# Optimization experiments

Measured on AMD Instinct MI355X. Metric: run time of the kernel, lower is better.

The kernel has to match this reference:

```python
import jax, jax.numpy as jnp
import numpy as np

B, T, H, D, V = 1, 512, 12, 64, 32000  # batch, seq, heads, head_dim, vocab


def setup_inputs() -> dict:
    key = jax.random.key(0)
    k0, k1, k2, k3 = jax.random.split(key, 4)
    x = jax.random.normal(k0, (B, T, H * D), dtype=jnp.float32)
    # per-head FFN weights: torch Linear(head_dim, head_dim) -> weight (out,in)=(D,D)
    W_ffn = jax.random.normal(k1, (H, D, D), dtype=jnp.float32) * 0.02
    b_ffn = jnp.zeros((H, D), dtype=jnp.float32)
    # per-head vocab attention: torch Linear(head_dim, vocab_size, bias=False) -> weight (V,D)
    W_vocab = jax.random.normal(k2, (H, V, D), dtype=jnp.float32) * 0.02
    temps = jnp.ones((H,), dtype=jnp.float32)
    # shared vocab embedding table (vocab_size, n_embd)
    E = jax.random.normal(k3, (V, H * D), dtype=jnp.float32) * 0.02
    return {"x": x, "W_ffn": W_ffn, "b_ffn": b_ffn, "W_vocab": W_vocab,
            "temps": temps, "E": E}


def reference(x, W_ffn, b_ffn, W_vocab, temps, E):
    Bx, Tx, C = x.shape
    Hn, Dn, _ = W_ffn.shape
    xh = x.reshape(Bx, Tx, Hn, Dn)                         # (B,T,H,D)
    # per-head FFN (Linear: y = x @ W^T + b)
    ffn = jnp.einsum('bthd,hed->bthe', xh, W_ffn) + b_ffn  # (B,T,H,D)
    # per-head vocab logits against weight bank (H,V,D)
    logits = jnp.einsum('bthd,hvd->bthv', ffn, W_vocab)    # (B,T,H,V)
    temp = jnp.maximum(temps, 0.1)[None, None, :, None]    # clamp(min=0.1)
    w = jax.nn.softmax(logits / temp, axis=-1)             # (B,T,H,V)
    # back-project through per-head slices of vocab embedding table
    Eh = E.reshape(E.shape[0], Hn, Dn)                     # (V,H,D)
    out = jnp.einsum('bthv,vhd->bthd', w, Eh)              # (B,T,H,D)
    # dropout is identity at eval (p used at train only)
    return out.reshape(Bx, Tx, C)
```

## Files before the change

### kernel.cpp

```cpp
#include <hip/hip_runtime.h>
#include <hip/hip_bf16.h>
#include <cstddef>

#define T_TOK 512
#define NH    12
#define HD    64
#define NV    32000
#define CEMB  768
#define NC    20
#define VC    (NV/NC)
#define NSUB  (VC/64)
#define QTILE 256
#define SK 72
#define SE 72
#define SP 72

typedef short v8bf __attribute__((ext_vector_type(8)));
typedef float v4f  __attribute__((ext_vector_type(4)));

__device__ __forceinline__ unsigned short f2bf(float f) {
    unsigned u = __float_as_uint(f);
    u += 0x7fffu + ((u >> 16) & 1u);
    return (unsigned short)(u >> 16);
}

__global__ void ffn_kernel(const float* __restrict__ x, const float* __restrict__ Wf,
                           const float* __restrict__ bf, const float* __restrict__ temps,
                           unsigned short* __restrict__ Qb) {
    const int t = blockIdx.x, h = blockIdx.y, e = threadIdx.x;
    __shared__ float xs[HD];
    xs[e] = x[t*CEMB + h*HD + e];
    __syncthreads();
    const float4* w4  = (const float4*)(Wf + (size_t)(h*HD + e)*HD);
    const float4* xs4 = (const float4*)xs;
    float acc = bf[h*HD + e];
    #pragma unroll
    for (int i = 0; i < HD/4; ++i) {
        float4 a = xs4[i], b = w4[i];
        acc += a.x*b.x + a.y*b.y + a.z*b.z + a.w*b.w;
    }
    float tau = temps[h]; tau = (tau < 0.1f) ? 0.1f : tau;
    Qb[((size_t)h*T_TOK + t)*HD + e] = f2bf(acc / tau);
}

__global__ __launch_bounds__(256) void e_transpose(const float* __restrict__ E,
                                                   unsigned short* __restrict__ ET) {
    const int v0 = blockIdx.x * 64, h = blockIdx.y;
    const int tid = threadIdx.x;
    __shared__ float Ts[64*65];
    #pragma unroll
    for (int r = 0; r < 4; ++r) {
        int f = tid + 256*r, v = f >> 4, d4 = f & 15;
        float4 e4 = *(const float4*)&E[(size_t)(v0 + v)*CEMB + h*HD + d4*4];
        Ts[(d4*4+0)*65 + v] = e4.x;
        Ts[(d4*4+1)*65 + v] = e4.y;
        Ts[(d4*4+2)*65 + v] = e4.z;
        Ts[(d4*4+3)*65 + v] = e4.w;
    }
    __syncthreads();
    #pragma unroll
    for (int r = 0; r < 2; ++r) {
        int u = tid + 256*r, d = u >> 3, c16 = u & 7;
        const float* row = &Ts[d*65 + c16*8];
        uint4 w;
        w.x = f2bf(row[0]) | ((unsigned)f2bf(row[1]) << 16);
        w.y = f2bf(row[2]) | ((unsigned)f2bf(row[3]) << 16);
        w.z = f2bf(row[4]) | ((unsigned)f2bf(row[5]) << 16);
        w.w = f2bf(row[6]) | ((unsigned)f2bf(row[7]) << 16);
        *(uint4*)&ET[(size_t)(h*64 + d)*NV + v0 + c16*8] = w;
    }
}

__global__ __launch_bounds__(256, 2) void flash_mfma(
        const unsigned short* __restrict__ Qb, const float* __restrict__ Wv,
        const unsigned short* __restrict__ ET, float* __restrict__ Npart,
        float* __restrict__ Zpart) {
    const int c = blockIdx.x, qg = blockIdx.y, h = blockIdx.z;
    const int tid  = threadIdx.x;
    const int wq   = tid >> 6;
    const int l    = tid & 63;
    const int l15  = l & 15, quad = l >> 4;

    __shared__ unsigned short Ks[64*SK];
    __shared__ unsigned short Es[64*SE];
    __shared__ unsigned short Ps[QTILE*SP];

    const int tbase = qg*QTILE + wq*64;

    v8bf qf[4][2];
    #pragma unroll
    for (int nt = 0; nt < 4; ++nt)
        #pragma unroll
        for (int kb = 0; kb < 2; ++kb)
            qf[nt][kb] = *(const v8bf*)&Qb[((size_t)h*T_TOK + tbase + nt*16 + l15)*HD
                                           + kb*32 + quad*8];

    v4f o[4][4];
    #pragma unroll
    for (int mt = 0; mt < 4; ++mt)
        #pragma unroll
        for (int nt = 0; nt < 4; ++nt) { v4f z; z[0]=0.f;z[1]=0.f;z[2]=0.f;z[3]=0.f; o[mt][nt]=z; }
    float zacc[4] = {0.f, 0.f, 0.f, 0.f};

    const float*          Kg = Wv + ((size_t)h*NV + (size_t)c*VC)*HD;
    const unsigned short* Eg = ET + (size_t)h*64*NV + (size_t)c*VC;

    for (int s = 0; s < NSUB; ++s) {
        const float4* kgp = (const float4*)(Kg + (size_t)s*64*HD);
        #pragma unroll
        for (int r = 0; r < 4; ++r) {
            float4 kv = kgp[tid + 256*r];
            int f = tid + 256*r, v = f >> 4, d4 = f & 15;
            uint2 w;
            w.x = f2bf(kv.x) | ((unsigned)f2bf(kv.y) << 16);
            w.y = f2bf(kv.z) | ((unsigned)f2bf(kv.w) << 16);
            *(uint2*)&Ks[v*SK + d4*4] = w;
        }
        #pragma unroll
        for (int r = 0; r < 2; ++r) {
            int u = tid + 256*r, d = u >> 3, c16 = u & 7;
            uint4 ev = *(const uint4*)&Eg[(size_t)d*NV + s*64 + c16*8];
            *(uint4*)&Es[d*SE + c16*8] = ev;
        }
        __syncthreads();

        v8bf kf[4][2];
        #pragma unroll
        for (int mt = 0; mt < 4; ++mt)
            #pragma unroll
            for (int kb = 0; kb < 2; ++kb)
                kf[mt][kb] = *(const v8bf*)&Ks[(mt*16 + l15)*SK + kb*32 + quad*8];

        #pragma unroll
        for (int nt = 0; nt < 4; ++nt) {
            #pragma unroll
            for (int mt = 0; mt < 4; ++mt) {
                v4f sa; sa[0]=0.f; sa[1]=0.f; sa[2]=0.f; sa[3]=0.f;
                sa = __builtin_amdgcn_mfma_f32_16x16x32_bf16(kf[mt][0], qf[nt][0], sa, 0, 0, 0);
                sa = __builtin_amdgcn_mfma_f32_16x16x32_bf16(kf[mt][1], qf[nt][1], sa, 0, 0, 0);
                float p0 = __expf(sa[0]), p1 = __expf(sa[1]);
                float p2 = __expf(sa[2]), p3 = __expf(sa[3]);
                zacc[nt] += (p0 + p1) + (p2 + p3);
                uint2 w;
                w.x = f2bf(p0) | ((unsigned)f2bf(p1) << 16);
                w.y = f2bf(p2) | ((unsigned)f2bf(p3) << 16);
                *(uint2*)&Ps[(wq*64 + nt*16 + l15)*SP + mt*16 + quad*4] = w;
            }
        }

        v8bf ef[4][2];
        #pragma unroll
        for (int mt = 0; mt < 4; ++mt)
            #pragma unroll
            for (int kb = 0; kb < 2; ++kb)
                ef[mt][kb] = *(const v8bf*)&Es[(mt*16 + l15)*SE + kb*32 + quad*8];

        #pragma unroll
        for (int nt = 0; nt < 4; ++nt) {
            const int prow = (wq*64 + nt*16 + l15)*SP;
            v8bf pf0 = *(const v8bf*)&Ps[prow + quad*8];
            v8bf pf1 = *(const v8bf*)&Ps[prow + 32 + quad*8];
            #pragma unroll
            for (int mt = 0; mt < 4; ++mt) {
                o[mt][nt] = __builtin_amdgcn_mfma_f32_16x16x32_bf16(ef[mt][0], pf0, o[mt][nt], 0, 0, 0);
                o[mt][nt] = __builtin_amdgcn_mfma_f32_16x16x32_bf16(ef[mt][1], pf1, o[mt][nt], 0, 0, 0);
            }
        }
        __syncthreads();
    }

    #pragma unroll
    for (int nt = 0; nt < 4; ++nt) {
        float z = zacc[nt];
        z += __shfl_xor(z, 16, 64);
        z += __shfl_xor(z, 32, 64);
        if (quad == 0)
            Zpart[((size_t)c*T_TOK + tbase + nt*16 + l15)*NH + h] = z;
    }
    #pragma unroll
    for (int nt = 0; nt < 4; ++nt) {
        const int t = tbase + nt*16 + l15;
        float* np = Npart + (((size_t)c*T_TOK + t)*NH + h)*HD;
        #pragma unroll
        for (int mt = 0; mt < 4; ++mt) {
            v4f ov = o[mt][nt];
            *(float4*)&np[mt*16 + quad*4] = make_float4(ov[0], ov[1], ov[2], ov[3]);
        }
    }
}

__global__ void combine_kernel(const float* __restrict__ Npart,
                               const float* __restrict__ Zpart,
                               float* __restrict__ out) {
    const int idx = blockIdx.x*256 + threadIdx.x;
    const int t = idx / CEMB;
    const int rem = idx % CEMB;
    const int h = rem / HD;
    float n = 0.f, z = 0.f;
    #pragma unroll
    for (int c = 0; c < NC; ++c) {
        n += Npart[(((size_t)c*T_TOK + t)*NH + h)*HD + (rem & 63)];
        z += Zpart[((size_t)c*T_TOK + t)*NH + h];
    }
    out[idx] = n / z;
}

extern "C" void kernel_launch(void* const* d_in, const int* in_sizes, int n_in,
                              void* d_out, int out_size, void* d_ws, size_t ws_size,
                              hipStream_t stream) {
    const float* x     = (const float*)d_in[0];
    const float* Wf    = (const float*)d_in[1];
    const float* bf    = (const float*)d_in[2];
    const float* Wv    = (const float*)d_in[3];
    const float* temps = (const float*)d_in[4];
    const float* E     = (const float*)d_in[5];
    float* out = (float*)d_out;

    char* ws = (char*)d_ws;
    float*          Npart = (float*)ws;
    float*          Zpart = (float*)(ws + 31457280);
    unsigned short* Qb    = (unsigned short*)(ws + 31948800);
    unsigned short* ET    = (unsigned short*)(ws + 32735232);

    e_transpose  <<<dim3(NV/64, NH),        256, 0, stream>>>(E, ET);
    ffn_kernel   <<<dim3(T_TOK, NH),         64, 0, stream>>>(x, Wf, bf, temps, Qb);
    flash_mfma   <<<dim3(NC, T_TOK/QTILE, NH), 256, 0, stream>>>(Qb, Wv, ET, Npart, Zpart);
    combine_kernel<<<dim3((T_TOK*CEMB)/256), 256, 0, stream>>>(Npart, Zpart, out);
}
```

Before: 325.0 us.

## Double-buffer flash loop with async LDS loads, XOR swizzle, bf16 partials

The main loop now double-buffers the K and E tiles, using global_load_lds for E and register prefetch for K, so loads overlap MFMA work and one barrier per iteration is removed. LDS padding is replaced by an XOR swizzle to avoid bank conflicts. The exponent switches to exp2 with log2e folded into Q, the vocab split grows from 20 to 50 chunks for more parallelism, and partial numerators are stored as bf16, with a combine kernel that handles two elements per thread. The costs are extra LDS, more partial traffic from the larger split, and reduced precision in the partial sums.

```diff
diff --git a/kernel.cpp b/kernel.cpp
--- a/kernel.cpp
+++ b/kernel.cpp
@@ -7,13 +7,11 @@
 #define HD    64
 #define NV    32000
 #define CEMB  768
-#define NC    20
+#define NC    50
 #define VC    (NV/NC)
 #define NSUB  (VC/64)
 #define QTILE 256
-#define SK 72
-#define SE 72
-#define SP 72
+#define LOG2E 1.44269504088896340736f
 
 typedef short v8bf __attribute__((ext_vector_type(8)));
 typedef float v4f  __attribute__((ext_vector_type(4)));
@@ -22,6 +20,17 @@
     unsigned u = __float_as_uint(f);
     u += 0x7fffu + ((u >> 16) & 1u);
     return (unsigned short)(u >> 16);
+}
+__device__ __forceinline__ unsigned pkbf(float a, float b) {
+    return (unsigned)f2bf(a) | ((unsigned)f2bf(b) << 16);
+}
+__device__ __forceinline__ float bf2f(unsigned short u) {
+    return __uint_as_float(((unsigned)u) << 16);
+}
+__device__ __forceinline__ void gld16(const void* g, void* l) {
+    __builtin_amdgcn_global_load_lds(
+        (const __attribute__((address_space(1))) unsigned*)g,
+        (__attribute__((address_space(3))) unsigned*)l, 16, 0, 0);
 }
 
 __global__ void ffn_kernel(const float* __restrict__ x, const float* __restrict__ Wf,
@@ -40,7 +49,7 @@
         acc += a.x*b.x + a.y*b.y + a.z*b.z + a.w*b.w;
     }
     float tau = temps[h]; tau = (tau < 0.1f) ? 0.1f : tau;
-    Qb[((size_t)h*T_TOK + t)*HD + e] = f2bf(acc / tau);
+    Qb[((size_t)h*T_TOK + t)*HD + e] = f2bf(acc * LOG2E / tau);
 }
 
 __global__ __launch_bounds__(256) void e_transpose(const float* __restrict__ E,
@@ -63,27 +72,28 @@
         int u = tid + 256*r, d = u >> 3, c16 = u & 7;
         const float* row = &Ts[d*65 + c16*8];
         uint4 w;
-        w.x = f2bf(row[0]) | ((unsigned)f2bf(row[1]) << 16);
-        w.y = f2bf(row[2]) | ((unsigned)f2bf(row[3]) << 16);
-        w.z = f2bf(row[4]) | ((unsigned)f2bf(row[5]) << 16);
-        w.w = f2bf(row[6]) | ((unsigned)f2bf(row[7]) << 16);
+        w.x = pkbf(row[0], row[1]);
+        w.y = pkbf(row[2], row[3]);
+        w.z = pkbf(row[4], row[5]);
+        w.w = pkbf(row[6], row[7]);
         *(uint4*)&ET[(size_t)(h*64 + d)*NV + v0 + c16*8] = w;
     }
 }
 
 __global__ __launch_bounds__(256, 2) void flash_mfma(
         const unsigned short* __restrict__ Qb, const float* __restrict__ Wv,
-        const unsigned short* __restrict__ ET, float* __restrict__ Npart,
+        const unsigned short* __restrict__ ET, unsigned short* __restrict__ Npart,
         float* __restrict__ Zpart) {
     const int c = blockIdx.x, qg = blockIdx.y, h = blockIdx.z;
     const int tid  = threadIdx.x;
     const int wq   = tid >> 6;
-    const int l    = tid & 63;
-    const int l15  = l & 15, quad = l >> 4;
-
-    __shared__ unsigned short Ks[64*SK];
-    __shared__ unsigned short Es[64*SE];
-    __shared__ unsigned short Ps[QTILE*SP];
+    const int lane = tid & 63;
+    const int l15  = lane & 15, quad = lane >> 4;
+    const int X    = l15 & 7;
+
+    __shared__ unsigned short Kb[2][64*64];
+    __shared__ unsigned short Eb[2][64*64];
+    __shared__ unsigned short Ps[QTILE*64];
 
     const int tbase = qg*QTILE + wq*64;
 
@@ -99,74 +109,99 @@
     #pragma unroll
     for (int mt = 0; mt < 4; ++mt)
         #pragma unroll
-        for (int nt = 0; nt < 4; ++nt) { v4f z; z[0]=0.f;z[1]=0.f;z[2]=0.f;z[3]=0.f; o[mt][nt]=z; }
+        for (int nt = 0; nt < 4; ++nt) { v4f z = {0.f,0.f,0.f,0.f}; o[mt][nt] = z; }
     float zacc[4] = {0.f, 0.f, 0.f, 0.f};
 
-    const float*          Kg = Wv + ((size_t)h*NV + (size_t)c*VC)*HD;
-    const unsigned short* Eg = ET + (size_t)h*64*NV + (size_t)c*VC;
-
+    const int kv = wq*16 + (lane >> 2);
+    const int Xk = kv & 7;
+    const float* kgl = Wv + ((size_t)h*NV + (size_t)c*VC + kv)*HD + (lane & 3)*4;
+    int kwoff[4];
+    #pragma unroll
+    for (int r = 0; r < 4; ++r)
+        kwoff[r] = kv*64 + (((((lane&3)>>1) + 2*r) ^ Xk))*8 + (lane&1)*4;
+    const int Gv = (lane & 7) ^ (lane >> 3);
+    const unsigned short* eg0 = ET + (size_t)(h*64 + wq*16 + (lane >> 3))*NV
+                                   + (size_t)c*VC + Gv*8;
+    const unsigned short* eg1 = eg0 + (size_t)8*NV;
+
+    {
+        gld16(eg0, &Eb[0][(wq*16)*64]);
+        gld16(eg1, &Eb[0][(wq*16 + 8)*64]);
+        float4 k0[4];
+        #pragma unroll
+        for (int r = 0; r < 4; ++r) k0[r] = *(const float4*)(kgl + r*16);
+        #pragma unroll
+        for (int r = 0; r < 4; ++r) {
+            uint2 w = { pkbf(k0[r].x, k0[r].y), pkbf(k0[r].z, k0[r].w) };
+            *(uint2*)&Kb[0][kwoff[r]] = w;
+        }
+        __syncthreads();
+    }
+
+    int nb = 1;
     for (int s = 0; s < NSUB; ++s) {
-        const float4* kgp = (const float4*)(Kg + (size_t)s*64*HD);
-        #pragma unroll
-        for (int r = 0; r < 4; ++r) {
-            float4 kv = kgp[tid + 256*r];
-            int f = tid + 256*r, v = f >> 4, d4 = f & 15;
-            uint2 w;
-            w.x = f2bf(kv.x) | ((unsigned)f2bf(kv.y) << 16);
-            w.y = f2bf(kv.z) | ((unsigned)f2bf(kv.w) << 16);
-            *(uint2*)&Ks[v*SK + d4*4] = w;
-        }
-        #pragma unroll
-        for (int r = 0; r < 2; ++r) {
-            int u = tid + 256*r, d = u >> 3, c16 = u & 7;
-            uint4 ev = *(const uint4*)&Eg[(size_t)d*NV + s*64 + c16*8];
-            *(uint4*)&Es[d*SE + c16*8] = ev;
-        }
-        __syncthreads();
+        const int cur = nb ^ 1;
+        const bool pre = (s + 1 < NSUB);
+        float4 kr[4];
+        if (pre) {
+            gld16(eg0 + (s+1)*64, &Eb[nb][(wq*16)*64]);
+            gld16(eg1 + (s+1)*64, &Eb[nb][(wq*16 + 8)*64]);
+            #pragma unroll
+            for (int r = 0; r < 4; ++r)
+                kr[r] = *(const float4*)(kgl + (size_t)(s+1)*4096 + r*16);
+        }
 
         v8bf kf[4][2];
         #pragma unroll
-        for (int mt = 0; mt < 4; ++mt)
-            #pragma unroll
-            for (int kb = 0; kb < 2; ++kb)
-                kf[mt][kb] = *(const v8bf*)&Ks[(mt*16 + l15)*SK + kb*32 + quad*8];
-
+        for (int mt = 0; mt < 4; ++mt) {
+            const int row = (mt*16 + l15)*64;
+            kf[mt][0] = *(const v8bf*)&Kb[cur][row + ((quad     ^ X))*8];
+            kf[mt][1] = *(const v8bf*)&Kb[cur][row + (((4+quad) ^ X))*8];
+        }
         #pragma unroll
         for (int nt = 0; nt < 4; ++nt) {
             #pragma unroll
             for (int mt = 0; mt < 4; ++mt) {
-                v4f sa; sa[0]=0.f; sa[1]=0.f; sa[2]=0.f; sa[3]=0.f;
+                v4f sa = {0.f,0.f,0.f,0.f};
                 sa = __builtin_amdgcn_mfma_f32_16x16x32_bf16(kf[mt][0], qf[nt][0], sa, 0, 0, 0);
                 sa = __builtin_amdgcn_mfma_f32_16x16x32_bf16(kf[mt][1], qf[nt][1], sa, 0, 0, 0);
-                float p0 = __expf(sa[0]), p1 = __expf(sa[1]);
-                float p2 = __expf(sa[2]), p3 = __expf(sa[3]);
+                float p0 = exp2f(sa[0]), p1 = exp2f(sa[1]);
+                float p2 = exp2f(sa[2]), p3 = exp2f(sa[3]);
                 zacc[nt] += (p0 + p1) + (p2 + p3);
-                uint2 w;
-                w.x = f2bf(p0) | ((unsigned)f2bf(p1) << 16);
-                w.y = f2bf(p2) | ((unsigned)f2bf(p3) << 16);
-                *(uint2*)&Ps[(wq*64 + nt*16 + l15)*SP + mt*16 + quad*4] = w;
+                uint2 w = { pkbf(p0, p1), pkbf(p2, p3) };
+                const int q = wq*64 + nt*16 + l15;
+                *(uint2*)&Ps[q*64 + (((mt*2 + (quad>>1)) ^ X))*8 + (quad&1)*4] = w;
             }
         }
 
         v8bf ef[4][2];
         #pragma unroll
-        for (int mt = 0; mt < 4; ++mt)
-            #pragma unroll
-            for (int kb = 0; kb < 2; ++kb)
-                ef[mt][kb] = *(const v8bf*)&Es[(mt*16 + l15)*SE + kb*32 + quad*8];
-
+        for (int mt = 0; mt < 4; ++mt) {
+            const int row = (mt*16 + l15)*64;
+            ef[mt][0] = *(const v8bf*)&Eb[cur][row + ((quad     ^ X))*8];
+            ef[mt][1] = *(const v8bf*)&Eb[cur][row + (((4+quad) ^ X))*8];
+        }
         #pragma unroll
         for (int nt = 0; nt < 4; ++nt) {
-            const int prow = (wq*64 + nt*16 + l15)*SP;
-            v8bf pf0 = *(const v8bf*)&Ps[prow + quad*8];
-            v8bf pf1 = *(const v8bf*)&Ps[prow + 32 + quad*8];
+            const int q = wq*64 + nt*16 + l15;
+            v8bf pf0 = *(const v8bf*)&Ps[q*64 + ((quad     ^ X))*8];
+            v8bf pf1 = *(const v8bf*)&Ps[q*64 + (((4+quad) ^ X))*8];
             #pragma unroll
             for (int mt = 0; mt < 4; ++mt) {
                 o[mt][nt] = __builtin_amdgcn_mfma_f32_16x16x32_bf16(ef[mt][0], pf0, o[mt][nt], 0, 0, 0);
                 o[mt][nt] = __builtin_amdgcn_mfma_f32_16x16x32_bf16(ef[mt][1], pf1, o[mt][nt], 0, 0, 0);
             }
         }
-        __syncthreads();
+
+        if (pre) {
+            #pragma unroll
+            for (int r = 0; r < 4; ++r) {
+                uint2 w = { pkbf(kr[r].x, kr[r].y), pkbf(kr[r].z, kr[r].w) };
+                *(uint2*)&Kb[nb][kwoff[r]] = w;
+            }
+            __syncthreads();
+        }
+        nb ^= 1;
     }
 
     #pragma unroll
@@ -180,29 +215,33 @@
     #pragma unroll
     for (int nt = 0; nt < 4; ++nt) {
         const int t = tbase + nt*16 + l15;
-        float* np = Npart + (((size_t)c*T_TOK + t)*NH + h)*HD;
+        unsigned short* np = Npart + (((size_t)c*T_TOK + t)*NH + h)*HD;
         #pragma unroll
         for (int mt = 0; mt < 4; ++mt) {
             v4f ov = o[mt][nt];
-            *(float4*)&np[mt*16 + quad*4] = make_float4(ov[0], ov[1], ov[2], ov[3]);
-        }
-    }
-}
-
-__global__ void combine_kernel(const float* __restrict__ Npart,
+            uint2 w = { pkbf(ov[0], ov[1]), pkbf(ov[2], ov[3]) };
+            *(uint2*)&np[mt*16 + quad*4] = w;
+        }
+    }
+}
+
+__global__ void combine_kernel(const unsigned short* __restrict__ Npart,
                                const float* __restrict__ Zpart,
                                float* __restrict__ out) {
-    const int idx = blockIdx.x*256 + threadIdx.x;
+    const int idx = (blockIdx.x*256 + threadIdx.x)*2;
     const int t = idx / CEMB;
     const int rem = idx % CEMB;
-    const int h = rem / HD;
-    float n = 0.f, z = 0.f;
+    const int h = rem >> 6, d = rem & 63;
+    float n0 = 0.f, n1 = 0.f, z = 0.f;
     #pragma unroll
     for (int c = 0; c < NC; ++c) {
-        n += Npart[(((size_t)c*T_TOK + t)*NH + h)*HD + (rem & 63)];
-        z += Zpart[((size_t)c*T_TOK + t)*NH + h];
-    }
-    out[idx] = n / z;
+        unsigned u = *(const unsigned*)&Npart[(((size_t)c*T_TOK + t)*NH + h)*HD + d];
+        n0 += bf2f((unsigned short)(u & 0xffffu));
+        n1 += bf2f((unsigned short)(u >> 16));
+        z  += Zpart[((size_t)c*T_TOK + t)*NH + h];
+    }
+    out[idx]   = n0 / z;
+    out[idx+1] = n1 / z;
 }
 
 extern "C" void kernel_launch(void* const* d_in, const int* in_sizes, int n_in,
@@ -217,13 +256,13 @@
     float* out = (float*)d_out;
 
     char* ws = (char*)d_ws;
-    float*          Npart = (float*)ws;
-    float*          Zpart = (float*)(ws + 31457280);
-    unsigned short* Qb    = (unsigned short*)(ws + 31948800);
-    unsigned short* ET    = (unsigned short*)(ws + 32735232);
-
-    e_transpose  <<<dim3(NV/64, NH),        256, 0, stream>>>(E, ET);
-    ffn_kernel   <<<dim3(T_TOK, NH),         64, 0, stream>>>(x, Wf, bf, temps, Qb);
-    flash_mfma   <<<dim3(NC, T_TOK/QTILE, NH), 256, 0, stream>>>(Qb, Wv, ET, Npart, Zpart);
-    combine_kernel<<<dim3((T_TOK*CEMB)/256), 256, 0, stream>>>(Npart, Zpart, out);
-}
+    unsigned short* Npart = (unsigned short*)ws;
+    float*          Zpart = (float*)(ws + 39321600);
+    unsigned short* Qb    = (unsigned short*)(ws + 40550400);
+    unsigned short* ET    = (unsigned short*)(ws + 41336832);
+
+    e_transpose   <<<dim3(NV/64, NH),          256, 0, stream>>>(E, ET);
+    ffn_kernel    <<<dim3(T_TOK, NH),           64, 0, stream>>>(x, Wf, bf, temps, Qb);
+    flash_mfma    <<<dim3(NC, T_TOK/QTILE, NH), 256, 0, stream>>>(Qb, Wv, ET, Npart, Zpart);
+    combine_kernel<<<dim3((T_TOK*CEMB)/512),   256, 0, stream>>>(Npart, Zpart, out);
+}
```

Result: no change. 323.4 us (-0.5%).
